# Optimization experiments

Hardware: AMD Instinct MI355X
Metric: run time of the kernel (lower is better)

The kernel has to match this reference:

```python
import jax, jax.numpy as jnp
import numpy as np

H = 512      # hidden_dim
OPS = 12     # num_ops
E = 112      # total_edges = num_cells * sum(i+2 for i in range(num_nodes)) = 8*14


def setup_inputs() -> dict:
    key = jax.random.key(0)
    ks = jax.random.split(key, 16)
    s = lambda k, shape: jax.random.normal(k, shape, dtype=jnp.float32) * 0.05
    return {
        "temperature": 1,
        "h0": s(ks[0], (2, H)),
        "c0": s(ks[1], (2, H)),
        "Wih0": s(ks[2], (4 * H, H)),
        "Whh0": s(ks[3], (4 * H, H)),
        "bih0": s(ks[4], (4 * H,)),
        "bhh0": s(ks[5], (4 * H,)),
        "Wih1": s(ks[6], (4 * H, H)),
        "Whh1": s(ks[7], (4 * H, H)),
        "bih1": s(ks[8], (4 * H,)),
        "bhh1": s(ks[9], (4 * H,)),
        "emb": s(ks[10], (OPS, H)),
        "cW1": s(ks[11], (E, H, H)),
        "cb1": s(ks[12], (E, H)),
        "cW2": s(ks[13], (E, H, OPS)),
        "cb2": s(ks[14], (E, OPS)),
    }


def _lstm_cell(x, h, c, Wih, Whh, bih, bhh):
    # PyTorch LSTM gate order: i, f, g, o
    gates = x @ Wih.T + bih + h @ Whh.T + bhh  # [4H]
    i, f, g, o = jnp.split(gates, 4)
    c2 = jax.nn.sigmoid(f) * c + jax.nn.sigmoid(i) * jnp.tanh(g)
    h2 = jax.nn.sigmoid(o) * jnp.tanh(c2)
    return h2, c2


def reference(temperature, h0, c0, Wih0, Whh0, bih0, bhh0,
              Wih1, Whh1, bih1, bhh1, emb, cW1, cb1, cW2, cb2):
    temp = jnp.asarray(temperature, jnp.float32)
    # Gumbel-max trick == torch Categorical sampling (fixed on-device noise)
    gumbel = jax.random.gumbel(jax.random.key(42), (E, OPS), dtype=jnp.float32)

    def step(carry, xs):
        h, c, prev_action = carry          # h, c: [2, H]
        idx, W1, b1, W2, b2, gnoise = xs
        x = jnp.where(idx == 0, jnp.zeros((H,), jnp.float32), emb[prev_action])
        h0n, c0n = _lstm_cell(x, h[0], c[0], Wih0, Whh0, bih0, bhh0)
        h1n, c1n = _lstm_cell(h0n, h[1], c[1], Wih1, Whh1, bih1, bhh1)
        hmlp = jax.nn.relu(h1n @ W1 + b1)   # controller hidden
        logits = (hmlp @ W2 + b2) / temp    # [OPS]
        logp = jax.nn.log_softmax(logits)
        action = jnp.argmax(logits + gnoise).astype(jnp.int32)
        lp = logp[action]
        ent = -jnp.sum(jnp.exp(logp) * logp)
        new_carry = (jnp.stack([h0n, h1n]), jnp.stack([c0n, c1n]), action)
        return new_carry, (action, lp, ent)

    init = (h0, c0, jnp.int32(0))
    xs = (jnp.arange(E), cW1, cb1, cW2, cb2, gumbel)
    _, (actions, log_probs, entropies) = jax.lax.scan(step, init, xs)
    return actions, log_probs, entropies
```

## Files before the change

kernel.cpp:

```cpp
#include <hip/hip_runtime.h>
#include <math.h>

#define H    512
#define OPS  12
#define E    112
#define NWG  128
#define NT   256

typedef unsigned long long u64;
typedef unsigned int u32x4 __attribute__((ext_vector_type(4)));

#define TW_HB0   0
#define TW_HB1   1024
#define TW_HMB   2048
#define TW_TOTAL 3072

#define SW(j) (((j) & ~31) | (((j) + ((((j) >> 5) & 7) << 2)) & 31))

__device__ __forceinline__ float sigf(float x) { return 1.f / (1.f + expf(-x)); }

__device__ __forceinline__ void threefry_42(unsigned x0, unsigned x1,
                                            unsigned& o0, unsigned& o1) {
  const unsigned k0 = 0u, k1 = 42u;
  const unsigned k2 = k0 ^ k1 ^ 0x1BD11BDAu;
  x0 += k0; x1 += k1;
#define TF_R(rot) { x0 += x1; x1 = (x1 << rot) | (x1 >> (32 - rot)); x1 ^= x0; }
  TF_R(13) TF_R(15) TF_R(26) TF_R(6)
  x0 += k1; x1 += k2 + 1u;
  TF_R(17) TF_R(29) TF_R(16) TF_R(24)
  x0 += k2; x1 += k0 + 2u;
  TF_R(13) TF_R(15) TF_R(26) TF_R(6)
  x0 += k0; x1 += k1 + 3u;
  TF_R(17) TF_R(29) TF_R(16) TF_R(24)
  x0 += k1; x1 += k2 + 4u;
  TF_R(13) TF_R(15) TF_R(26) TF_R(6)
  x0 += k2; x1 += k0 + 5u;
#undef TF_R
  o0 = x0; o1 = x1;
}

__device__ __forceinline__ float bits_to_gumbel(unsigned bits) {
  unsigned fb = (bits >> 9) | 0x3f800000u;
  float u = __uint_as_float(fb) - 1.0f;
  u = u + 1.17549435e-38f;
  u = fmaxf(1.17549435e-38f, u);
  return -logf(-logf(u));
}

__device__ __forceinline__ float decode_temp(const void* temp_p) {
  float tf = *(const float*)temp_p;
  float a = fabsf(tf);
  if (a > 1e-6f && a < 1e6f) return tf;
  int ti = *(const int*)temp_p;
  if (ti != 0 && ti > -1000000 && ti < 1000000) return (float)ti;
  double td = *(const double*)temp_p;
  double ad = fabs(td);
  if (ad > 1e-6 && ad < 1e6) return (float)td;
  return 1.0f;
}

__device__ __forceinline__ void tag_store(u64* p, unsigned tag, float f) {
  u64 v = ((u64)tag << 32) | (u64)__float_as_uint(f);
  __hip_atomic_store(p, v, __ATOMIC_RELAXED, __HIP_MEMORY_SCOPE_SYSTEM);
}
__device__ __forceinline__ void tag_poll2(const u64* p, unsigned tag,
                                          float& f0, float& f1) {
  u32x4 v;
  for (;;) {
    asm volatile("global_load_dwordx4 %0, %1, off sc0 sc1\n\t"
                 "s_waitcnt vmcnt(0)"
                 : "=&v"(v) : "v"(p) : "memory");
    if (v.y == tag && v.w == tag) break;
    __builtin_amdgcn_s_sleep(1);
  }
  f0 = __uint_as_float(v.x);
  f1 = __uint_as_float(v.z);
}

__global__ void k_init(u64* tw) {
  int t = blockIdx.x * blockDim.x + threadIdx.x;
  if (t < TW_TOTAL) tw[t] = 0ull;
}
__global__ void k_diag(float* out, float v) {
  if (threadIdx.x == 0 && blockIdx.x == 0) out[0] = v;
}

__global__ void __launch_bounds__(NT)
policy_persist(const void* temp_p,
               const float* __restrict__ h0_in, const float* __restrict__ c0_in,
               const float* __restrict__ Wih0,  const float* __restrict__ Whh0,
               const float* __restrict__ bih0,  const float* __restrict__ bhh0,
               const float* __restrict__ Wih1,  const float* __restrict__ Whh1,
               const float* __restrict__ bih1,  const float* __restrict__ bhh1,
               const float* __restrict__ emb,   const float* __restrict__ cW1,
               const float* __restrict__ cb1,   const float* __restrict__ cW2,
               const float* __restrict__ cb2,
               float* __restrict__ out, float* ws) {
  __shared__ __align__(16) float h0full[H], shp1[H], hm[H];
  __shared__ float g0pre[16], g1bpre[16], g1loc[16];
  __shared__ float ewloc[12 * 16], b0loc[16], b1loc[16];
  __shared__ float gum[E * OPS];
  __shared__ float w1s[512 * 5];
  __shared__ float w2s[512 * 13];
  __shared__ float c0loc[4], c1loc[4];
  __shared__ float spart[4][4];

  const int tid = threadIdx.x;
  const int bid = blockIdx.x;
  const int j0  = bid * 4;
  const int cb  = (bid & 7) * 16 + (bid >> 3);
  const float invt = 1.f / decode_temp(temp_p);

  u64* HB0 = (u64*)(ws + 16) + TW_HB0;
  u64* HB1 = (u64*)(ws + 16) + TW_HB1;
  u64* HMB = (u64*)(ws + 16) + TW_HMB;

  for (int p = tid; p < E * OPS; p += NT) {
    unsigned y0, y1;
    threefry_42(0u, (unsigned)p, y0, y1);
    gum[p] = bits_to_gumbel(y0 ^ y1);
  }
  for (int j = tid; j < H; j += NT) {
    h0full[SW(j)] = h0_in[j];
    shp1[SW(j)]   = h0_in[H + j];
  }
  if (tid < 192) {
    int a = tid / 16, ridx = tid % 16;
    int g = ridx >> 2, dj = ridx & 3;
    int row = g * H + j0 + dj;
    const float* er = emb + a * H;
    const float* wr = Wih0 + (size_t)row * H;
    float acc = 0.f;
    for (int k = 0; k < H; k += 4) {
      float4 e4 = *(const float4*)(er + k);
      float4 w4 = *(const float4*)(wr + k);
      acc += e4.x * w4.x + e4.y * w4.y + e4.z * w4.z + e4.w * w4.w;
    }
    ewloc[tid] = acc;
  }
  if (tid < 16) {
    int g = tid >> 2, dj = tid & 3;
    int row = g * H + j0 + dj;
    b0loc[tid] = bih0[row] + bhh0[row];
    b1loc[tid] = bih1[row] + bhh1[row];
  }
  if (tid < 4) {
    c0loc[tid] = c0_in[j0 + tid];
    c1loc[tid] = c0_in[H + j0 + tid];
  }
  __syncthreads();

  {
    int rowidx = tid >> 3, lane = tid & 7;
    int cell = rowidx >> 4, ridx = rowidx & 15;
    int g = ridx >> 2, dj = ridx & 3;
    int row = g * H + j0 + dj;
    const float* wr = (cell ? Whh1 : Whh0) + (size_t)row * H + lane * 64;
    const float* hv = cell ? shp1 : h0full;
    float acc = 0.f;
#pragma unroll
    for (int k = 0; k < 64; k += 4) {
      float4 w4 = *(const float4*)(wr + k);
      float4 h4 = *(const float4*)&hv[SW(lane * 64 + k)];
      acc += w4.x * h4.x + w4.y * h4.y + w4.z * h4.z + w4.w * h4.w;
    }
    acc += __shfl_xor(acc, 1);
    acc += __shfl_xor(acc, 2);
    acc += __shfl_xor(acc, 4);
    if (lane == 0) {
      if (cell == 0) g0pre[ridx] = acc + b0loc[ridx];
      else           g1bpre[ridx] = acc;
    }
    const float* wb = cW1 + (size_t)cb * 4;
    float4 r0 = *(const float4*)(wb + (size_t)tid * H);
    float4 r1 = *(const float4*)(wb + (size_t)(tid + 256) * H);
    int k0 = tid * 5, k1 = (tid + 256) * 5;
    w1s[k0] = r0.x; w1s[k0 + 1] = r0.y; w1s[k0 + 2] = r0.z; w1s[k0 + 3] = r0.w;
    w1s[k1] = r1.x; w1s[k1 + 1] = r1.y; w1s[k1 + 2] = r1.z; w1s[k1 + 3] = r1.w;
  }
  __syncthreads();

#pragma unroll 1
  for (int i = 0; i < E; ++i) {
    const int p = i & 1;
    const unsigned tg = (unsigned)(i + 1);

    if (i > 0) {
      const int q = (i - 1) & 1;
      int t2 = tid * 2;
      tag_poll2(&HMB[q * 512 + t2], (unsigned)i, hm[t2], hm[t2 + 1]);
      __syncthreads();
      if (tid < 64) {
        float lg[OPS];
#pragma unroll
        for (int o = 0; o < OPS; ++o) lg[o] = 0.f;
#pragma unroll
        for (int jj = 0; jj < 8; ++jj) {
          int j = jj * 64 + tid;
          float hmv = hm[j];
          const float* w2r = &w2s[j * 13];
#pragma unroll
          for (int o = 0; o < OPS; ++o) lg[o] += hmv * w2r[o];
        }
#pragma unroll
        for (int s = 1; s < 64; s <<= 1) {
#pragma unroll
          for (int o = 0; o < OPS; ++o) lg[o] += __shfl_xor(lg[o], s);
        }
#pragma unroll
        for (int o = 0; o < OPS; ++o) lg[o] = (lg[o] + cb2[(i - 1) * OPS + o]) * invt;
        float best = -1e30f; int act = 0;
#pragma unroll
        for (int o = 0; o < OPS; ++o) {
          float v = lg[o] + gum[(i - 1) * OPS + o];
          if (v > best) { best = v; act = o; }
        }
        if (tid < 4) {
          float gi = g0pre[tid]      + ewloc[act * 16 + tid];
          float gf = g0pre[4 + tid]  + ewloc[act * 16 + 4 + tid];
          float gg = g0pre[8 + tid]  + ewloc[act * 16 + 8 + tid];
          float go = g0pre[12 + tid] + ewloc[act * 16 + 12 + tid];
          float cn = sigf(gf) * c0loc[tid] + sigf(gi) * tanhf(gg);
          c0loc[tid] = cn;
          tag_store(&HB0[p * 512 + j0 + tid], tg, sigf(go) * tanhf(cn));
        }
        if (bid == 0) {
          float mx = lg[0];
#pragma unroll
          for (int o = 1; o < OPS; ++o) mx = fmaxf(mx, lg[o]);
          float se = 0.f;
#pragma unroll
          for (int o = 0; o < OPS; ++o) se += expf(lg[o] - mx);
          float logZ = mx + logf(se);
          if (tid == 0) {
            float lp = lg[act] - logZ;
            float ent = 0.f;
            for (int o = 0; o < OPS; ++o) {
              float l2 = lg[o] - logZ;
              ent -= expf(l2) * l2;
            }
            out[i - 1]         = (float)act;
            out[E + i - 1]     = lp;
            out[2 * E + i - 1] = ent;
          }
        }
      }
    } else {
      if (tid < 4) {
        float gi = g0pre[tid];
        float gf = g0pre[4 + tid];
        float gg = g0pre[8 + tid];
        float go = g0pre[12 + tid];
        float cn = sigf(gf) * c0loc[tid] + sigf(gi) * tanhf(gg);
        c0loc[tid] = cn;
        tag_store(&HB0[p * 512 + j0 + tid], tg, sigf(go) * tanhf(cn));
      }
    }

    {
      int t2 = tid * 2;
      int sw = SW(t2);
      tag_poll2(&HB0[p * 512 + t2], tg, h0full[sw], h0full[sw + 1]);
    }
    __syncthreads();

    {
      int ridx = tid >> 4, lane = tid & 15;
      int g = ridx >> 2, dj = ridx & 3;
      int row = g * H + j0 + dj;
      const float* wr = Wih1 + (size_t)row * H + lane * 32;
      float acc = 0.f;
#pragma unroll
      for (int k = 0; k < 32; k += 4) {
        float4 w4 = *(const float4*)(wr + k);
        float4 h4 = *(const float4*)&h0full[SW(lane * 32 + k)];
        acc += w4.x * h4.x + w4.y * h4.y + w4.z * h4.z + w4.w * h4.w;
      }
      acc += __shfl_xor(acc, 1);
      acc += __shfl_xor(acc, 2);
      acc += __shfl_xor(acc, 4);
      acc += __shfl_xor(acc, 8);
      if (lane == 0) g1loc[ridx] = acc + g1bpre[ridx] + b1loc[ridx];
    }
    __syncthreads();

    if (tid < 4) {
      float gi = g1loc[tid];
      float gf = g1loc[4 + tid];
      float gg = g1loc[8 + tid];
      float go = g1loc[12 + tid];
      float cn = sigf(gf) * c1loc[tid] + sigf(gi) * tanhf(gg);
      c1loc[tid] = cn;
      tag_store(&HB1[p * 512 + j0 + tid], tg, sigf(go) * tanhf(cn));
    }

    float4 v0, v1;
    if (i + 1 < E) {
      const float* wb = cW1 + (size_t)(i + 1) * H * H + (size_t)cb * 4;
      v0 = *(const float4*)(wb + (size_t)tid * H);
      v1 = *(const float4*)(wb + (size_t)(tid + 256) * H);
    }
    if (tid < 128) {
      int ridx = tid >> 3, lane = tid & 7;
      int g = ridx >> 2, dj = ridx & 3;
      int row = g * H + j0 + dj;
      const float* wr = Whh0 + (size_t)row * H + lane * 64;
      float acc = 0.f;
#pragma unroll
      for (int k = 0; k < 64; k += 4) {
        float4 w4 = *(const float4*)(wr + k);
        float4 h4 = *(const float4*)&h0full[SW(lane * 64 + k)];
        acc += w4.x * h4.x + w4.y * h4.y + w4.z * h4.z + w4.w * h4.w;
      }
      acc += __shfl_xor(acc, 1);
      acc += __shfl_xor(acc, 2);
      acc += __shfl_xor(acc, 4);
      if (lane == 0) g0pre[ridx] = acc + b0loc[ridx];
    }
    {
      const float* wsrc = cW2 + (size_t)i * H * OPS;
#pragma unroll
      for (int rr = 0; rr < 2; ++rr) {
        int r = tid * 2 + rr;
        const float* s = wsrc + r * 12;
        float4 a = *(const float4*)(s);
        float4 b = *(const float4*)(s + 4);
        float4 c = *(const float4*)(s + 8);
        float* d = &w2s[r * 13];
        d[0] = a.x; d[1] = a.y; d[2]  = a.z; d[3]  = a.w;
        d[4] = b.x; d[5] = b.y; d[6]  = b.z; d[7]  = b.w;
        d[8] = c.x; d[9] = c.y; d[10] = c.z; d[11] = c.w;
      }
    }

    {
      int t2 = tid * 2;
      int sw = SW(t2);
      tag_poll2(&HB1[p * 512 + t2], tg, shp1[sw], shp1[sw + 1]);
    }
    __syncthreads();

    {
      int wv = tid >> 6, ln = tid & 63;
      int jl = ln & 3, ks = ln >> 2;
      int kbase = wv * 128 + ks * 8;
      float acc = 0.f;
#pragma unroll
      for (int t = 0; t < 8; ++t) {
        int k = kbase + t;
        acc += shp1[SW(k)] * w1s[k * 5 + jl];
      }
      acc += __shfl_xor(acc, 4);
      acc += __shfl_xor(acc, 8);
      acc += __shfl_xor(acc, 16);
      acc += __shfl_xor(acc, 32);
      if (ln < 4) spart[wv][ln] = acc;
    }
    __syncthreads();
    if (tid < 4) {
      float s = spart[0][tid] + spart[1][tid] + spart[2][tid] + spart[3][tid];
      s += cb1[(size_t)i * H + cb * 4 + tid];
      tag_store(&HMB[p * 512 + cb * 4 + tid], tg, fmaxf(s, 0.f));
    }

    if (i + 1 < E) {
      if (tid < 128) {
        int ridx = tid >> 3, lane = tid & 7;
        int g = ridx >> 2, dj = ridx & 3;
        int row = g * H + j0 + dj;
        const float* wr = Whh1 + (size_t)row * H + lane * 64;
        float acc = 0.f;
#pragma unroll
        for (int k = 0; k < 64; k += 4) {
          float4 w4 = *(const float4*)(wr + k);
          float4 h4 = *(const float4*)&shp1[SW(lane * 64 + k)];
          acc += w4.x * h4.x + w4.y * h4.y + w4.z * h4.z + w4.w * h4.w;
        }
        acc += __shfl_xor(acc, 1);
        acc += __shfl_xor(acc, 2);
        acc += __shfl_xor(acc, 4);
        if (lane == 0) g1bpre[ridx] = acc;
      }
      int k0 = tid * 5, k1 = (tid + 256) * 5;
      w1s[k0] = v0.x; w1s[k0 + 1] = v0.y; w1s[k0 + 2] = v0.z; w1s[k0 + 3] = v0.w;
      w1s[k1] = v1.x; w1s[k1 + 1] = v1.y; w1s[k1 + 2] = v1.z; w1s[k1 + 3] = v1.w;
    }
  }

  if (bid == 0) {
    const int q = (E - 1) & 1;
    int t2 = tid * 2;
    tag_poll2(&HMB[q * 512 + t2], (unsigned)E, hm[t2], hm[t2 + 1]);
    __syncthreads();
    if (tid < 64) {
      float lg[OPS];
#pragma unroll
      for (int o = 0; o < OPS; ++o) lg[o] = 0.f;
#pragma unroll
      for (int jj = 0; jj < 8; ++jj) {
        int j = jj * 64 + tid;
        float hmv = hm[j];
        const float* w2r = &w2s[j * 13];
#pragma unroll
        for (int o = 0; o < OPS; ++o) lg[o] += hmv * w2r[o];
      }
#pragma unroll
      for (int s = 1; s < 64; s <<= 1) {
#pragma unroll
        for (int o = 0; o < OPS; ++o) lg[o] += __shfl_xor(lg[o], s);
      }
#pragma unroll
      for (int o = 0; o < OPS; ++o) lg[o] = (lg[o] + cb2[(E - 1) * OPS + o]) * invt;
      float mx = lg[0];
#pragma unroll
      for (int o = 1; o < OPS; ++o) mx = fmaxf(mx, lg[o]);
      float se = 0.f;
#pragma unroll
      for (int o = 0; o < OPS; ++o) se += expf(lg[o] - mx);
      float logZ = mx + logf(se);
      float best = -1e30f; int act = 0;
#pragma unroll
      for (int o = 0; o < OPS; ++o) {
        float v = lg[o] + gum[(E - 1) * OPS + o];
        if (v > best) { best = v; act = o; }
      }
      if (tid == 0) {
        float lp = lg[act] - logZ;
        float ent = 0.f;
        for (int o = 0; o < OPS; ++o) {
          float l2 = lg[o] - logZ;
          ent -= expf(l2) * l2;
        }
        out[E - 1]     = (float)act;
        out[2 * E - 1] = lp;
        out[3 * E - 1] = ent;
      }
    }
  }
}

extern "C" void kernel_launch(void* const* d_in, const int* in_sizes, int n_in,
                              void* d_out, int out_size, void* d_ws, size_t ws_size,
                              hipStream_t stream) {
  (void)out_size; (void)ws_size;
  float* out = (float*)d_out;
  float* ws  = (float*)d_ws;

  (void)hipGetLastError();

  static const long long expect[16] = {
      1, 1024, 1024, 1048576, 1048576, 2048, 2048,
      1048576, 1048576, 2048, 2048, 6144,
      29360128, 57344, 688128, 1344 };
  int bad = -1;
  if (n_in != 16) bad = 99;
  else {
    for (int i = 0; i < 16; ++i)
      if ((long long)in_sizes[i] != expect[i]) { bad = i; break; }
  }

  k_init<<<12, 256, 0, stream>>>((u64*)(ws + 16));
  if (bad >= 0) {
    k_diag<<<1, 64, 0, stream>>>(out, 80000.0f + (float)bad);
    return;
  }

  policy_persist<<<NWG, NT, 0, stream>>>(
      d_in[0],
      (const float*)d_in[1],  (const float*)d_in[2],
      (const float*)d_in[3],  (const float*)d_in[4],
      (const float*)d_in[5],  (const float*)d_in[6],
      (const float*)d_in[7],  (const float*)d_in[8],
      (const float*)d_in[9],  (const float*)d_in[10],
      (const float*)d_in[11], (const float*)d_in[12],
      (const float*)d_in[13], (const float*)d_in[14],
      (const float*)d_in[15],
      out, ws);

  hipError_t e = hipGetLastError();
  if (e != hipSuccess) {
    k_diag<<<1, 64, 0, stream>>>(out, 90000.0f + (float)(int)e);
  }
}
```

Measured before the change: 1.083 ms.

## Replace hidden-MLP broadcast with atomic logit accumulation and counter barrier

Each workgroup now multiplies its four hidden-MLP outputs by its slice of W2 and atomically adds its 12 partial logits into a rotating global buffer, then bumps a global counter. Consumers wait on that counter and read 12 logits instead of polling 512 tagged hidden values and recomputing the full W2 product in every workgroup. This removes the per-step reload of the full W2 slice into shared memory and the redundant 512x12 reduction done by all 128 workgroups. In exchange it adds global float atomics and a single-counter barrier. Float atomic summation order also makes the logits nondeterministic, which could flip argmax ties.

```diff
diff --git a/kernel.cpp b/kernel.cpp
--- a/kernel.cpp
+++ b/kernel.cpp
@@ -12,8 +12,8 @@
 
 #define TW_HB0   0
 #define TW_HB1   1024
-#define TW_HMB   2048
-#define TW_TOTAL 3072
+#define TW_TOTAL 2048
+#define LG_F     (16 + 2 * TW_TOTAL)
 
 #define SW(j) (((j) & ~31) | (((j) + ((((j) >> 5) & 7) << 2)) & 31))
 
@@ -77,9 +77,10 @@
   f1 = __uint_as_float(v.z);
 }
 
-__global__ void k_init(u64* tw) {
+__global__ void k_init(u64* tw, unsigned* cnt) {
   int t = blockIdx.x * blockDim.x + threadIdx.x;
-  if (t < TW_TOTAL) tw[t] = 0ull;
+  if (t < TW_TOTAL + 24) tw[t] = 0ull;
+  if (t == 0) *cnt = 0u;
 }
 __global__ void k_diag(float* out, float v) {
   if (threadIdx.x == 0 && blockIdx.x == 0) out[0] = v;
@@ -96,12 +97,14 @@
                const float* __restrict__ cb1,   const float* __restrict__ cW2,
                const float* __restrict__ cb2,
                float* __restrict__ out, float* ws) {
-  __shared__ __align__(16) float h0full[H], shp1[H], hm[H];
+  __shared__ __align__(16) float h0full[H], shp1[H];
   __shared__ float g0pre[16], g1bpre[16], g1loc[16];
   __shared__ float ewloc[12 * 16], b0loc[16], b1loc[16];
-  __shared__ float gum[E * OPS];
+  __shared__ float gum[E * OPS], cbl[E * OPS];
   __shared__ float w1s[512 * 5];
-  __shared__ float w2s[512 * 13];
+  __shared__ float w2row[4][OPS];
+  __shared__ float plg[4][OPS];
+  __shared__ float lgs[OPS];
   __shared__ float c0loc[4], c1loc[4];
   __shared__ float spart[4][4];
 
@@ -113,12 +116,14 @@
 
   u64* HB0 = (u64*)(ws + 16) + TW_HB0;
   u64* HB1 = (u64*)(ws + 16) + TW_HB1;
-  u64* HMB = (u64*)(ws + 16) + TW_HMB;
+  float*    LG  = ws + LG_F;
+  unsigned* cnt = (unsigned*)(ws + 8);
 
   for (int p = tid; p < E * OPS; p += NT) {
     unsigned y0, y1;
     threefry_42(0u, (unsigned)p, y0, y1);
     gum[p] = bits_to_gumbel(y0 ^ y1);
+    cbl[p] = cb2[p];
   }
   for (int j = tid; j < H; j += NT) {
     h0full[SW(j)] = h0_in[j];
@@ -147,6 +152,13 @@
   if (tid < 4) {
     c0loc[tid] = c0_in[j0 + tid];
     c1loc[tid] = c0_in[H + j0 + tid];
+    const float* wsrc = cW2 + (size_t)(cb * 4 + tid) * OPS;
+    float4 a = *(const float4*)(wsrc);
+    float4 b = *(const float4*)(wsrc + 4);
+    float4 c = *(const float4*)(wsrc + 8);
+    w2row[tid][0] = a.x; w2row[tid][1] = a.y; w2row[tid][2]  = a.z; w2row[tid][3]  = a.w;
+    w2row[tid][4] = b.x; w2row[tid][5] = b.y; w2row[tid][6]  = b.z; w2row[tid][7]  = b.w;
+    w2row[tid][8] = c.x; w2row[tid][9] = c.y; w2row[tid][10] = c.z; w2row[tid][11] = c.w;
   }
   __syncthreads();
 
@@ -186,64 +198,51 @@
     const unsigned tg = (unsigned)(i + 1);
 
     if (i > 0) {
-      const int q = (i - 1) & 1;
-      int t2 = tid * 2;
-      tag_poll2(&HMB[q * 512 + t2], (unsigned)i, hm[t2], hm[t2 + 1]);
+      const unsigned tgt = 128u * (unsigned)i;
+      while (__hip_atomic_load(cnt, __ATOMIC_RELAXED,
+                               __HIP_MEMORY_SCOPE_SYSTEM) < tgt)
+        __builtin_amdgcn_s_sleep(1);
+      if (tid < OPS) {
+        lgs[tid] = __hip_atomic_load(&LG[((i - 1) & 3) * OPS + tid],
+                                     __ATOMIC_RELAXED, __HIP_MEMORY_SCOPE_SYSTEM);
+      }
       __syncthreads();
-      if (tid < 64) {
-        float lg[OPS];
-#pragma unroll
-        for (int o = 0; o < OPS; ++o) lg[o] = 0.f;
-#pragma unroll
-        for (int jj = 0; jj < 8; ++jj) {
-          int j = jj * 64 + tid;
-          float hmv = hm[j];
-          const float* w2r = &w2s[j * 13];
-#pragma unroll
-          for (int o = 0; o < OPS; ++o) lg[o] += hmv * w2r[o];
+      float lgv[OPS];
+#pragma unroll
+      for (int o = 0; o < OPS; ++o)
+        lgv[o] = (lgs[o] + cbl[(i - 1) * OPS + o]) * invt;
+      float best = -1e30f; int act = 0;
+#pragma unroll
+      for (int o = 0; o < OPS; ++o) {
+        float v = lgv[o] + gum[(i - 1) * OPS + o];
+        if (v > best) { best = v; act = o; }
+      }
+      if (tid < 4) {
+        float gi = g0pre[tid]      + ewloc[act * 16 + tid];
+        float gf = g0pre[4 + tid]  + ewloc[act * 16 + 4 + tid];
+        float gg = g0pre[8 + tid]  + ewloc[act * 16 + 8 + tid];
+        float go = g0pre[12 + tid] + ewloc[act * 16 + 12 + tid];
+        float cn = sigf(gf) * c0loc[tid] + sigf(gi) * tanhf(gg);
+        c0loc[tid] = cn;
+        tag_store(&HB0[p * 512 + j0 + tid], tg, sigf(go) * tanhf(cn));
+      }
+      if (bid == 0 && tid == 0) {
+        float mx = lgv[0];
+#pragma unroll
+        for (int o = 1; o < OPS; ++o) mx = fmaxf(mx, lgv[o]);
+        float se = 0.f;
+#pragma unroll
+        for (int o = 0; o < OPS; ++o) se += expf(lgv[o] - mx);
+        float logZ = mx + logf(se);
+        float lp = lgv[act] - logZ;
+        float ent = 0.f;
+        for (int o = 0; o < OPS; ++o) {
+          float l2 = lgv[o] - logZ;
+          ent -= expf(l2) * l2;
         }
-#pragma unroll
-        for (int s = 1; s < 64; s <<= 1) {
-#pragma unroll
-          for (int o = 0; o < OPS; ++o) lg[o] += __shfl_xor(lg[o], s);
-        }
-#pragma unroll
-        for (int o = 0; o < OPS; ++o) lg[o] = (lg[o] + cb2[(i - 1) * OPS + o]) * invt;
-        float best = -1e30f; int act = 0;
-#pragma unroll
-        for (int o = 0; o < OPS; ++o) {
-          float v = lg[o] + gum[(i - 1) * OPS + o];
-          if (v > best) { best = v; act = o; }
-        }
-        if (tid < 4) {
-          float gi = g0pre[tid]      + ewloc[act * 16 + tid];
-          float gf = g0pre[4 + tid]  + ewloc[act * 16 + 4 + tid];
-          float gg = g0pre[8 + tid]  + ewloc[act * 16 + 8 + tid];
-          float go = g0pre[12 + tid] + ewloc[act * 16 + 12 + tid];
-          float cn = sigf(gf) * c0loc[tid] + sigf(gi) * tanhf(gg);
-          c0loc[tid] = cn;
-          tag_store(&HB0[p * 512 + j0 + tid], tg, sigf(go) * tanhf(cn));
-        }
-        if (bid == 0) {
-          float mx = lg[0];
-#pragma unroll
-          for (int o = 1; o < OPS; ++o) mx = fmaxf(mx, lg[o]);
-          float se = 0.f;
-#pragma unroll
-          for (int o = 0; o < OPS; ++o) se += expf(lg[o] - mx);
-          float logZ = mx + logf(se);
-          if (tid == 0) {
-            float lp = lg[act] - logZ;
-            float ent = 0.f;
-            for (int o = 0; o < OPS; ++o) {
-              float l2 = lg[o] - logZ;
-              ent -= expf(l2) * l2;
-            }
-            out[i - 1]         = (float)act;
-            out[E + i - 1]     = lp;
-            out[2 * E + i - 1] = ent;
-          }
-        }
+        out[i - 1]         = (float)act;
+        out[E + i - 1]     = lp;
+        out[2 * E + i - 1] = ent;
       }
     } else {
       if (tid < 4) {
@@ -317,21 +316,6 @@
       acc += __shfl_xor(acc, 4);
       if (lane == 0) g0pre[ridx] = acc + b0loc[ridx];
     }
-    {
-      const float* wsrc = cW2 + (size_t)i * H * OPS;
-#pragma unroll
-      for (int rr = 0; rr < 2; ++rr) {
-        int r = tid * 2 + rr;
-        const float* s = wsrc + r * 12;
-        float4 a = *(const float4*)(s);
-        float4 b = *(const float4*)(s + 4);
-        float4 c = *(const float4*)(s + 8);
-        float* d = &w2s[r * 13];
-        d[0] = a.x; d[1] = a.y; d[2]  = a.z; d[3]  = a.w;
-        d[4] = b.x; d[5] = b.y; d[6]  = b.z; d[7]  = b.w;
-        d[8] = c.x; d[9] = c.y; d[10] = c.z; d[11] = c.w;
-      }
-    }
 
     {
       int t2 = tid * 2;
@@ -360,7 +344,24 @@
     if (tid < 4) {
       float s = spart[0][tid] + spart[1][tid] + spart[2][tid] + spart[3][tid];
       s += cb1[(size_t)i * H + cb * 4 + tid];
-      tag_store(&HMB[p * 512 + cb * 4 + tid], tg, fmaxf(s, 0.f));
+      float hmv = fmaxf(s, 0.f);
+#pragma unroll
+      for (int o = 0; o < OPS; ++o) plg[tid][o] = hmv * w2row[tid][o];
+    }
+    __syncthreads();
+    if (bid == 0 && i >= 2 && tid < OPS) {
+      __hip_atomic_store(&LG[((i - 2) & 3) * OPS + tid], 0.f,
+                         __ATOMIC_RELAXED, __HIP_MEMORY_SCOPE_SYSTEM);
+    }
+    if (tid < OPS) {
+      float ps = ((plg[0][tid] + plg[1][tid]) + plg[2][tid]) + plg[3][tid];
+      (void)__hip_atomic_fetch_add(&LG[(i & 3) * OPS + tid], ps,
+                                   __ATOMIC_RELAXED, __HIP_MEMORY_SCOPE_SYSTEM);
+    }
+    asm volatile("s_waitcnt vmcnt(0)" ::: "memory");
+    if (tid == 0) {
+      (void)__hip_atomic_fetch_add(cnt, 1u, __ATOMIC_RELAXED,
+                                   __HIP_MEMORY_SCOPE_SYSTEM);
     }
 
     if (i + 1 < E) {
@@ -384,57 +385,55 @@
       int k0 = tid * 5, k1 = (tid + 256) * 5;
       w1s[k0] = v0.x; w1s[k0 + 1] = v0.y; w1s[k0 + 2] = v0.z; w1s[k0 + 3] = v0.w;
       w1s[k1] = v1.x; w1s[k1 + 1] = v1.y; w1s[k1 + 2] = v1.z; w1s[k1 + 3] = v1.w;
+      if (tid < 4) {
+        const float* wsrc = cW2 + ((size_t)(i + 1) * H + cb * 4 + tid) * OPS;
+        float4 a = *(const float4*)(wsrc);
+        float4 b = *(const float4*)(wsrc + 4);
+        float4 c = *(const float4*)(wsrc + 8);
+        w2row[tid][0] = a.x; w2row[tid][1] = a.y; w2row[tid][2]  = a.z; w2row[tid][3]  = a.w;
+        w2row[tid][4] = b.x; w2row[tid][5] = b.y; w2row[tid][6]  = b.z; w2row[tid][7]  = b.w;
+        w2row[tid][8] = c.x; w2row[tid][9] = c.y; w2row[tid][10] = c.z; w2row[tid][11] = c.w;
+      }
     }
   }
 
   if (bid == 0) {
-    const int q = (E - 1) & 1;
-    int t2 = tid * 2;
-    tag_poll2(&HMB[q * 512 + t2], (unsigned)E, hm[t2], hm[t2 + 1]);
-    __syncthreads();
-    if (tid < 64) {
-      float lg[OPS];
-#pragma unroll
-      for (int o = 0; o < OPS; ++o) lg[o] = 0.f;
-#pragma unroll
-      for (int jj = 0; jj < 8; ++jj) {
-        int j = jj * 64 + tid;
-        float hmv = hm[j];
-        const float* w2r = &w2s[j * 13];
-#pragma unroll
-        for (int o = 0; o < OPS; ++o) lg[o] += hmv * w2r[o];
-      }
-#pragma unroll
-      for (int s = 1; s < 64; s <<= 1) {
-#pragma unroll
-        for (int o = 0; o < OPS; ++o) lg[o] += __shfl_xor(lg[o], s);
-      }
-#pragma unroll
-      for (int o = 0; o < OPS; ++o) lg[o] = (lg[o] + cb2[(E - 1) * OPS + o]) * invt;
-      float mx = lg[0];
-#pragma unroll
-      for (int o = 1; o < OPS; ++o) mx = fmaxf(mx, lg[o]);
+    const unsigned tgt = 128u * (unsigned)E;
+    while (__hip_atomic_load(cnt, __ATOMIC_RELAXED,
+                             __HIP_MEMORY_SCOPE_SYSTEM) < tgt)
+      __builtin_amdgcn_s_sleep(1);
+    if (tid < OPS) {
+      lgs[tid] = __hip_atomic_load(&LG[((E - 1) & 3) * OPS + tid],
+                                   __ATOMIC_RELAXED, __HIP_MEMORY_SCOPE_SYSTEM);
+    }
+    __syncthreads();
+    if (tid == 0) {
+      float lgv[OPS];
+#pragma unroll
+      for (int o = 0; o < OPS; ++o)
+        lgv[o] = (lgs[o] + cbl[(E - 1) * OPS + o]) * invt;
+      float best = -1e30f; int act = 0;
+#pragma unroll
+      for (int o = 0; o < OPS; ++o) {
+        float v = lgv[o] + gum[(E - 1) * OPS + o];
+        if (v > best) { best = v; act = o; }
+      }
+      float mx = lgv[0];
+#pragma unroll
+      for (int o = 1; o < OPS; ++o) mx = fmaxf(mx, lgv[o]);
       float se = 0.f;
 #pragma unroll
-      for (int o = 0; o < OPS; ++o) se += expf(lg[o] - mx);
+      for (int o = 0; o < OPS; ++o) se += expf(lgv[o] - mx);
       float logZ = mx + logf(se);
-      float best = -1e30f; int act = 0;
-#pragma unroll
+      float lp = lgv[act] - logZ;
+      float ent = 0.f;
       for (int o = 0; o < OPS; ++o) {
-        float v = lg[o] + gum[(E - 1) * OPS + o];
-        if (v > best) { best = v; act = o; }
-      }
-      if (tid == 0) {
-        float lp = lg[act] - logZ;
-        float ent = 0.f;
-        for (int o = 0; o < OPS; ++o) {
-          float l2 = lg[o] - logZ;
-          ent -= expf(l2) * l2;
-        }
-        out[E - 1]     = (float)act;
-        out[2 * E - 1] = lp;
-        out[3 * E - 1] = ent;
-      }
+        float l2 = lgv[o] - logZ;
+        ent -= expf(l2) * l2;
+      }
+      out[E - 1]     = (float)act;
+      out[2 * E - 1] = lp;
+      out[3 * E - 1] = ent;
     }
   }
 }
@@ -459,7 +458,7 @@
       if ((long long)in_sizes[i] != expect[i]) { bad = i; break; }
   }
 
-  k_init<<<12, 256, 0, stream>>>((u64*)(ws + 16));
+  k_init<<<12, 256, 0, stream>>>((u64*)(ws + 16), (unsigned*)(ws + 8));
   if (bad >= 0) {
     k_diag<<<1, 64, 0, stream>>>(out, 80000.0f + (float)bad);
     return;
```

Result: slower. 1.555 ms (+43.5%).
